# Kernel optimization log

Hardware: AMD Instinct MI355X
Metric: run time of the kernel (lower is better)

Reference implementation:

```python
import jax, jax.numpy as jnp
import numpy as np

B, S, D_IN, D_OUT = 4, 2048, 1024, 1024

def setup_inputs() -> dict:
    key = jax.random.key(0)
    k0, k1, k2, k3 = jax.random.split(key, 4)
    sc = 1.0 / np.sqrt(D_IN)
    return {
        "x": jax.random.normal(k0, (B, S, D_IN), dtype=jnp.float32),
        "wq": jax.random.normal(k1, (D_OUT, D_IN), dtype=jnp.float32) * sc,
        "wk": jax.random.normal(k2, (D_OUT, D_IN), dtype=jnp.float32) * sc,
        "wv": jax.random.normal(k3, (D_OUT, D_IN), dtype=jnp.float32) * sc,
    }

def reference(x, wq, wk, wv):
    # Linear (no bias): y = x @ W.T, W shaped [d_out, d_in]
    q = jnp.einsum("bsd,ed->bse", x, wq)
    k = jnp.einsum("bsd,ed->bse", x, wk)
    v = jnp.einsum("bsd,ed->bse", x, wv)
    scores = jnp.einsum("bqe,bke->bqk", q, k)  # [B,S,S]
    n = x.shape[1]
    causal = jnp.triu(jnp.ones((n, n), dtype=bool), k=1)  # True above diagonal -> masked
    scores = jnp.where(causal, -jnp.inf, scores)
    attn = jax.nn.softmax(scores / jnp.sqrt(jnp.asarray(k.shape[-1], scores.dtype)), axis=-1)
    # dropout p=0.0 -> identity
    return jnp.einsum("bqk,bke->bqe", attn, v)
```

## Files before the change

kernel.cpp:

```cpp
#include <hip/hip_runtime.h>

#define Bb 4
#define Ss 2048
#define Dd 1024

typedef unsigned short u16;
typedef __bf16 bf16x8 __attribute__((ext_vector_type(8)));
typedef float  f32x4  __attribute__((ext_vector_type(4)));

__device__ inline u16 f2bf(float f) {
  union { float f; unsigned u; } x; x.f = f;
  unsigned u = x.u;
  return (u16)((u + 0x7fffu + ((u >> 16) & 1u)) >> 16);
}

__device__ static inline void gl_lds16(const u16* g, u16* l) {
  __builtin_amdgcn_global_load_lds((__attribute__((address_space(1))) const void*)g,
                                   (__attribute__((address_space(3))) void*)l,
                                   16, 0, 0);
}

__global__ __launch_bounds__(256) void cast_kernel(const float* __restrict__ in,
                                                   u16* __restrict__ out, int n) {
  int i = (blockIdx.x * 256 + threadIdx.x) * 4;
  if (i >= n) return;
  float4 v = *(const float4*)(in + i);
  unsigned p0 = (unsigned)f2bf(v.x) | ((unsigned)f2bf(v.y) << 16);
  unsigned p1 = (unsigned)f2bf(v.z) | ((unsigned)f2bf(v.w) << 16);
  uint2 p; p.x = p0; p.y = p1;
  *(uint2*)(out + i) = p;
}

__global__ __launch_bounds__(256) void cast3_kernel(const float* __restrict__ w0,
                                                    const float* __restrict__ w1,
                                                    const float* __restrict__ w2,
                                                    u16* __restrict__ out) {
  const float* src = (blockIdx.y == 0) ? w0 : (blockIdx.y == 1) ? w1 : w2;
  u16* dst = out + (size_t)blockIdx.y * Dd * Dd;
  int i = (blockIdx.x * 256 + threadIdx.x) * 4;
  float4 v = *(const float4*)(src + i);
  unsigned p0 = (unsigned)f2bf(v.x) | ((unsigned)f2bf(v.y) << 16);
  unsigned p1 = (unsigned)f2bf(v.z) | ((unsigned)f2bf(v.w) << 16);
  uint2 p; p.x = p0; p.y = p1;
  *(uint2*)(dst + i) = p;
}

#define BM 128
#define BN 128
#define BK 32

__device__ inline void gemm_tile(const u16* __restrict__ A, int lda,
                                 const u16* __restrict__ Bp, int ldb,
                                 int kBeg, int kEnd,
                                 u16* lA, u16* lB, f32x4 acc[4][4]) {
  const int tid  = threadIdx.x;
  const int lane = tid & 63, wave = tid >> 6;
  const int quad = lane >> 4, r16 = lane & 15;
  const int wm = (wave & 1) * 64, wn = (wave >> 1) * 64;

  for (int k0 = kBeg; k0 < kEnd; k0 += BK) {
    __syncthreads();
#pragma unroll
    for (int q = 0; q < 2; q++) {
      int s = q * 256 + tid;
      int row = s >> 2, part = s & 3;
      gl_lds16(A + (size_t)row * lda + k0 + part * 8, lA + s * 8);
    }
#pragma unroll
    for (int q = 0; q < 2; q++) {
      int s = q * 256 + tid;
      int row = s >> 2, part = s & 3;
      gl_lds16(Bp + (size_t)row * ldb + k0 + part * 8, lB + s * 8);
    }
    __syncthreads();
    bf16x8 fa[4], fb[4];
#pragma unroll
    for (int t = 0; t < 4; t++)
      fa[t] = *(const bf16x8*)(lA + (wm + t * 16 + r16) * 32 + quad * 8);
#pragma unroll
    for (int t = 0; t < 4; t++)
      fb[t] = *(const bf16x8*)(lB + (wn + t * 16 + r16) * 32 + quad * 8);
#pragma unroll
    for (int tm = 0; tm < 4; tm++)
#pragma unroll
      for (int tn = 0; tn < 4; tn++)
        acc[tm][tn] = __builtin_amdgcn_mfma_f32_16x16x32_bf16(fa[tm], fb[tn],
                                                              acc[tm][tn], 0, 0, 0);
  }
}

__global__ __launch_bounds__(256) void qkv_gemm(const u16* __restrict__ xb,
                                                const u16* __restrict__ wb,
                                                u16* __restrict__ qkv) {
  __shared__ __align__(16) u16 lA[BM * 32];
  __shared__ __align__(16) u16 lB[BN * 32];
  const int zi = blockIdx.z;
  const int row0 = blockIdx.y * BM;
  const int col0 = blockIdx.x * BN;
  const u16* A  = xb + (size_t)row0 * Dd;
  const u16* Bp = wb + (size_t)zi * Dd * Dd + (size_t)col0 * Dd;
  f32x4 acc[4][4];
  const f32x4 zero = {0.f, 0.f, 0.f, 0.f};
#pragma unroll
  for (int tm = 0; tm < 4; tm++)
#pragma unroll
    for (int tn = 0; tn < 4; tn++) acc[tm][tn] = zero;

  gemm_tile(A, Dd, Bp, Dd, 0, Dd, lA, lB, acc);

  u16* out = qkv + (size_t)zi * ((size_t)Bb * Ss * Dd);
  const int lane = threadIdx.x & 63, wave = threadIdx.x >> 6;
  const int quad = lane >> 4, r16 = lane & 15;
  const int wm = (wave & 1) * 64, wn = (wave >> 1) * 64;
#pragma unroll
  for (int tm = 0; tm < 4; tm++)
#pragma unroll
    for (int tn = 0; tn < 4; tn++) {
      int rr = row0 + wm + tm * 16 + quad * 4;
      int cc = col0 + wn + tn * 16 + r16;
#pragma unroll
      for (int r = 0; r < 4; r++)
        out[(size_t)(rr + r) * Dd + cc] = f2bf(acc[tm][tn][r]);
    }
}

__global__ __launch_bounds__(256) void scores_gemm(const u16* __restrict__ qb,
                                                   const u16* __restrict__ kb,
                                                   u16* __restrict__ sc) {
  const int jt = blockIdx.x, it = blockIdx.y, b = blockIdx.z;
  if (jt > it) return;
  __shared__ __align__(16) u16 lA[BM * 32];
  __shared__ __align__(16) u16 lB[BN * 32];
  const u16* A  = qb + (size_t)b * Ss * Dd + (size_t)it * BM * Dd;
  const u16* Bp = kb + (size_t)b * Ss * Dd + (size_t)jt * BN * Dd;
  f32x4 acc[4][4];
  const f32x4 zero = {0.f, 0.f, 0.f, 0.f};
#pragma unroll
  for (int tm = 0; tm < 4; tm++)
#pragma unroll
    for (int tn = 0; tn < 4; tn++) acc[tm][tn] = zero;

  gemm_tile(A, Dd, Bp, Dd, 0, Dd, lA, lB, acc);

  u16* out = sc + (size_t)b * Ss * Ss;
  const int lane = threadIdx.x & 63, wave = threadIdx.x >> 6;
  const int quad = lane >> 4, r16 = lane & 15;
  const int wm = (wave & 1) * 64, wn = (wave >> 1) * 64;
#pragma unroll
  for (int tm = 0; tm < 4; tm++)
#pragma unroll
    for (int tn = 0; tn < 4; tn++) {
      int rr = it * BM + wm + tm * 16 + quad * 4;
      int cc = jt * BN + wn + tn * 16 + r16;
#pragma unroll
      for (int r = 0; r < 4; r++) {
        u16 v = (cc <= rr + r) ? f2bf(__expf(acc[tm][tn][r] * 0.03125f)) : (u16)0;
        out[(size_t)(rr + r) * Ss + cc] = v;
      }
    }
}

__global__ __launch_bounds__(256) void rowsum_kernel(const u16* __restrict__ sc,
                                                     float* __restrict__ invl) {
  const int wave = threadIdx.x >> 6, lane = threadIdx.x & 63;
  const int rid = blockIdx.x * 4 + wave;
  const int b = rid >> 11, i = rid & 2047;
  const u16* row = sc + (size_t)b * Ss * Ss + (size_t)i * Ss;
  const int n8 = ((i >> 7) + 1) * 128;
  float s = 0.f;
  for (int j = lane * 8; j < n8; j += 512) {
    bf16x8 v = *(const bf16x8*)(row + j);
#pragma unroll
    for (int t = 0; t < 8; t++) s += (float)v[t];
  }
  for (int o = 32; o; o >>= 1) s += __shfl_xor(s, o);
  if (lane == 0) invl[rid] = 1.f / s;
}

__global__ __launch_bounds__(256) void transpose_v(const u16* __restrict__ vb,
                                                   u16* __restrict__ vt) {
  const int b = blockIdx.z;
  const int s0 = blockIdx.x * 64;
  const int e0 = blockIdx.y * 64;
  __shared__ __align__(16) u16 t[64][72];
  const int tid = threadIdx.x;
  const u16* src = vb + (size_t)b * Ss * Dd;
#pragma unroll
  for (int g = tid; g < 512; g += 256) {
    int row = g >> 3, part = g & 7;
    uint4 v = *(const uint4*)(src + (size_t)(s0 + row) * Dd + e0 + part * 8);
    const u16* pv = (const u16*)&v;
#pragma unroll
    for (int j = 0; j < 8; j++) t[part * 8 + j][row] = pv[j];
  }
  __syncthreads();
  u16* dst = vt + (size_t)b * Dd * Ss;
#pragma unroll
  for (int g = tid; g < 512; g += 256) {
    int e = g >> 3, part = g & 7;
    uint4 v = *(const uint4*)(&t[e][part * 8]);
    *(uint4*)(dst + (size_t)(e0 + e) * Ss + s0 + part * 8) = v;
  }
}

__global__ __launch_bounds__(256) void pv_gemm(const u16* __restrict__ sc,
                                               const u16* __restrict__ vt,
                                               const float* __restrict__ invl,
                                               float* __restrict__ out) {
  const int idx = blockIdx.x;
  const int it = 15 - (idx >> 5);
  const int rem = idx & 31;
  const int col0 = (rem & 7) * BN;
  const int b = rem >> 3;
  const int row0 = it * BM;
  __shared__ __align__(16) u16 lA[BM * 32];
  __shared__ __align__(16) u16 lB[BN * 32];
  const u16* A  = sc + (size_t)b * Ss * Ss + (size_t)row0 * Ss;
  const u16* Bp = vt + (size_t)b * Dd * Ss + (size_t)col0 * Ss;
  f32x4 acc[4][4];
  const f32x4 zero = {0.f, 0.f, 0.f, 0.f};
#pragma unroll
  for (int tm = 0; tm < 4; tm++)
#pragma unroll
    for (int tn = 0; tn < 4; tn++) acc[tm][tn] = zero;

  gemm_tile(A, Ss, Bp, Ss, 0, row0 + BM, lA, lB, acc);

  float* o = out + (size_t)b * Ss * Dd;
  const float* il = invl + (size_t)b * Ss;
  const int lane = threadIdx.x & 63, wave = threadIdx.x >> 6;
  const int quad = lane >> 4, r16 = lane & 15;
  const int wm = (wave & 1) * 64, wn = (wave >> 1) * 64;
#pragma unroll
  for (int tm = 0; tm < 4; tm++) {
    int rbase = row0 + wm + tm * 16 + quad * 4;
    float s0 = il[rbase], s1 = il[rbase + 1], s2 = il[rbase + 2], s3 = il[rbase + 3];
#pragma unroll
    for (int tn = 0; tn < 4; tn++) {
      int cc = col0 + wn + tn * 16 + r16;
      o[(size_t)(rbase + 0) * Dd + cc] = acc[tm][tn][0] * s0;
      o[(size_t)(rbase + 1) * Dd + cc] = acc[tm][tn][1] * s1;
      o[(size_t)(rbase + 2) * Dd + cc] = acc[tm][tn][2] * s2;
      o[(size_t)(rbase + 3) * Dd + cc] = acc[tm][tn][3] * s3;
    }
  }
}

extern "C" void kernel_launch(void* const* d_in, const int* in_sizes, int n_in,
                              void* d_out, int out_size, void* d_ws, size_t ws_size,
                              hipStream_t stream) {
  const float* x  = (const float*)d_in[0];
  const float* wq = (const float*)d_in[1];
  const float* wk = (const float*)d_in[2];
  const float* wv = (const float*)d_in[3];
  float* out = (float*)d_out;
  char* ws = (char*)d_ws;
  if (ws_size < 106987520u) return;

  u16* qkv  = (u16*)(ws);
  u16* sc   = (u16*)(ws + 50331648u);
  u16* xb   = (u16*)(ws + 83886080u);
  u16* vt   = xb;
  u16* wb   = (u16*)(ws + 100663296u);
  float* invl = (float*)(ws + 106954752u);

  const size_t nQ = (size_t)Bb * Ss * Dd;

  cast_kernel<<<8192, 256, 0, stream>>>(x, xb, (int)nQ);
  cast3_kernel<<<dim3(1024, 3), 256, 0, stream>>>(wq, wk, wv, wb);

  qkv_gemm<<<dim3(Dd / BN, (Bb * Ss) / BM, 3), 256, 0, stream>>>(xb, wb, qkv);
  scores_gemm<<<dim3(Ss / BN, Ss / BM, Bb), 256, 0, stream>>>(qkv, qkv + nQ, sc);
  rowsum_kernel<<<(Bb * Ss) / 4, 256, 0, stream>>>(sc, invl);
  transpose_v<<<dim3(Ss / 64, Dd / 64, Bb), 256, 0, stream>>>(qkv + 2 * nQ, vt);
  pv_gemm<<<512, 256, 0, stream>>>(sc, vt, invl, out);
}
```

Before: 273.7 us.

## Fuse cast kernels, fold rowsum and V-transpose into scores kernel, XCD-aware remap

Merges the x and weight cast kernels into one launch. The rowsum kernel is removed: row sums are now accumulated in the scores epilogue with shuffles and atomicAdd, after a memset of the sum buffer. The V transpose now runs as extra blocks inside the scores launch, and only the lower-triangular score tiles are launched. qkv_gemm and scores tiles are remapped so neighbouring tiles land on the same XCD for L2 reuse. This cuts launch count and avoids re-reading the scores matrix, at the cost of atomics and a per-element reciprocal in pv_gemm.

```diff
diff --git a/kernel.cpp b/kernel.cpp
--- a/kernel.cpp
+++ b/kernel.cpp
@@ -13,6 +13,10 @@
   unsigned u = x.u;
   return (u16)((u + 0x7fffu + ((u >> 16) & 1u)) >> 16);
 }
+__device__ inline float bf2f(u16 h) {
+  union { unsigned u; float f; } x; x.u = ((unsigned)h) << 16;
+  return x.f;
+}
 
 __device__ static inline void gl_lds16(const u16* g, u16* l) {
   __builtin_amdgcn_global_load_lds((__attribute__((address_space(1))) const void*)g,
@@ -20,24 +24,24 @@
                                    16, 0, 0);
 }
 
-__global__ __launch_bounds__(256) void cast_kernel(const float* __restrict__ in,
-                                                   u16* __restrict__ out, int n) {
-  int i = (blockIdx.x * 256 + threadIdx.x) * 4;
-  if (i >= n) return;
-  float4 v = *(const float4*)(in + i);
-  unsigned p0 = (unsigned)f2bf(v.x) | ((unsigned)f2bf(v.y) << 16);
-  unsigned p1 = (unsigned)f2bf(v.z) | ((unsigned)f2bf(v.w) << 16);
-  uint2 p; p.x = p0; p.y = p1;
-  *(uint2*)(out + i) = p;
-}
-
-__global__ __launch_bounds__(256) void cast3_kernel(const float* __restrict__ w0,
-                                                    const float* __restrict__ w1,
-                                                    const float* __restrict__ w2,
-                                                    u16* __restrict__ out) {
-  const float* src = (blockIdx.y == 0) ? w0 : (blockIdx.y == 1) ? w1 : w2;
-  u16* dst = out + (size_t)blockIdx.y * Dd * Dd;
-  int i = (blockIdx.x * 256 + threadIdx.x) * 4;
+__global__ __launch_bounds__(256) void cast_all(const float* __restrict__ x,
+                                                const float* __restrict__ wq,
+                                                const float* __restrict__ wk,
+                                                const float* __restrict__ wv,
+                                                u16* __restrict__ xb,
+                                                u16* __restrict__ wb) {
+  int id = blockIdx.x;
+  const float* src; u16* dst; int off;
+  if (id < 8192) {
+    src = x; dst = xb; off = id * 1024;
+  } else {
+    int wi = id - 8192;
+    int w = wi >> 10;
+    src = (w == 0) ? wq : (w == 1) ? wk : wv;
+    dst = wb + (size_t)w * Dd * Dd;
+    off = (wi & 1023) * 1024;
+  }
+  int i = off + threadIdx.x * 4;
   float4 v = *(const float4*)(src + i);
   unsigned p0 = (unsigned)f2bf(v.x) | ((unsigned)f2bf(v.y) << 16);
   unsigned p1 = (unsigned)f2bf(v.z) | ((unsigned)f2bf(v.w) << 16);
@@ -92,11 +96,17 @@
 __global__ __launch_bounds__(256) void qkv_gemm(const u16* __restrict__ xb,
                                                 const u16* __restrict__ wb,
                                                 u16* __restrict__ qkv) {
-  __shared__ __align__(16) u16 lA[BM * 32];
-  __shared__ __align__(16) u16 lB[BN * 32];
-  const int zi = blockIdx.z;
-  const int row0 = blockIdx.y * BM;
-  const int col0 = blockIdx.x * BN;
+  __shared__ __align__(16) u16 shmem[8192];
+  u16* lA = shmem;
+  u16* lB = shmem + 4096;
+  const int id  = blockIdx.x;
+  const int xcd = id & 7, j = id >> 3;
+  const int xt  = j & 7;
+  const int yl  = (j >> 3) & 7;
+  const int zi  = j >> 6;
+  const int y   = xcd * 8 + yl;
+  const int row0 = y * BM;
+  const int col0 = xt * BN;
   const u16* A  = xb + (size_t)row0 * Dd;
   const u16* Bp = wb + (size_t)zi * Dd * Dd + (size_t)col0 * Dd;
   f32x4 acc[4][4];
@@ -124,13 +134,55 @@
     }
 }
 
-__global__ __launch_bounds__(256) void scores_gemm(const u16* __restrict__ qb,
-                                                   const u16* __restrict__ kb,
-                                                   u16* __restrict__ sc) {
-  const int jt = blockIdx.x, it = blockIdx.y, b = blockIdx.z;
-  if (jt > it) return;
-  __shared__ __align__(16) u16 lA[BM * 32];
-  __shared__ __align__(16) u16 lB[BN * 32];
+__global__ __launch_bounds__(256) void scores_fused(const u16* __restrict__ qb,
+                                                    const u16* __restrict__ kb,
+                                                    const u16* __restrict__ vb,
+                                                    u16* __restrict__ sc,
+                                                    u16* __restrict__ vt,
+                                                    float* __restrict__ lsum) {
+  __shared__ __align__(16) u16 shmem[8192];
+  const int id = blockIdx.x;
+  const int tid = threadIdx.x;
+
+  if (id >= 544) {
+    const int t2 = id - 544;
+    const int b = t2 >> 7, rem = t2 & 127;
+    const int e = rem >> 3, g = rem & 7;
+    const u16* src = vb + (size_t)b * Ss * Dd;
+    u16* dst = vt + (size_t)b * Dd * Ss;
+    u16 (*t)[72] = (u16(*)[72])shmem;
+    for (int q4 = 0; q4 < 4; q4++) {
+      int s0 = (g * 4 + q4) * 64, e0 = e * 64;
+      if (q4) __syncthreads();
+#pragma unroll
+      for (int gg = tid; gg < 512; gg += 256) {
+        int row = gg >> 3, part = gg & 7;
+        uint4 v = *(const uint4*)(src + (size_t)(s0 + row) * Dd + e0 + part * 8);
+        const u16* pv = (const u16*)&v;
+#pragma unroll
+        for (int jj = 0; jj < 8; jj++) t[part * 8 + jj][row] = pv[jj];
+      }
+      __syncthreads();
+#pragma unroll
+      for (int gg = tid; gg < 512; gg += 256) {
+        int ee = gg >> 3, part = gg & 7;
+        uint4 v = *(const uint4*)(&t[ee][part * 8]);
+        *(uint4*)(dst + (size_t)(e0 + ee) * Ss + s0 + part * 8) = v;
+      }
+    }
+    return;
+  }
+
+  const int xcd = id & 7, j = id >> 3;
+  const int b = j / 17, tloc = j - b * 17;
+  const int t = xcd * 17 + tloc;
+  int it = (int)((sqrtf(8.f * (float)t + 1.f) - 1.f) * 0.5f);
+  while ((it + 1) * (it + 2) / 2 <= t) it++;
+  while (it * (it + 1) / 2 > t) it--;
+  const int jt = t - it * (it + 1) / 2;
+
+  u16* lA = shmem;
+  u16* lB = shmem + 4096;
   const u16* A  = qb + (size_t)b * Ss * Dd + (size_t)it * BM * Dd;
   const u16* Bp = kb + (size_t)b * Ss * Dd + (size_t)jt * BN * Dd;
   f32x4 acc[4][4];
@@ -143,78 +195,57 @@
   gemm_tile(A, Dd, Bp, Dd, 0, Dd, lA, lB, acc);
 
   u16* out = sc + (size_t)b * Ss * Ss;
-  const int lane = threadIdx.x & 63, wave = threadIdx.x >> 6;
+  float* lr = lsum + (size_t)b * Ss;
+  const int lane = tid & 63, wave = tid >> 6;
   const int quad = lane >> 4, r16 = lane & 15;
   const int wm = (wave & 1) * 64, wn = (wave >> 1) * 64;
 #pragma unroll
-  for (int tm = 0; tm < 4; tm++)
+  for (int tm = 0; tm < 4; tm++) {
+    float psum[4] = {0.f, 0.f, 0.f, 0.f};
 #pragma unroll
     for (int tn = 0; tn < 4; tn++) {
       int rr = it * BM + wm + tm * 16 + quad * 4;
       int cc = jt * BN + wn + tn * 16 + r16;
 #pragma unroll
       for (int r = 0; r < 4; r++) {
-        u16 v = (cc <= rr + r) ? f2bf(__expf(acc[tm][tn][r] * 0.03125f)) : (u16)0;
-        out[(size_t)(rr + r) * Ss + cc] = v;
+        float p = 0.f;
+        u16 h = 0;
+        if (cc <= rr + r) {
+          h = f2bf(__expf(acc[tm][tn][r] * 0.03125f));
+          p = bf2f(h);
+        }
+        out[(size_t)(rr + r) * Ss + cc] = h;
+        psum[r] += p;
       }
     }
-}
-
-__global__ __launch_bounds__(256) void rowsum_kernel(const u16* __restrict__ sc,
-                                                     float* __restrict__ invl) {
-  const int wave = threadIdx.x >> 6, lane = threadIdx.x & 63;
-  const int rid = blockIdx.x * 4 + wave;
-  const int b = rid >> 11, i = rid & 2047;
-  const u16* row = sc + (size_t)b * Ss * Ss + (size_t)i * Ss;
-  const int n8 = ((i >> 7) + 1) * 128;
-  float s = 0.f;
-  for (int j = lane * 8; j < n8; j += 512) {
-    bf16x8 v = *(const bf16x8*)(row + j);
-#pragma unroll
-    for (int t = 0; t < 8; t++) s += (float)v[t];
-  }
-  for (int o = 32; o; o >>= 1) s += __shfl_xor(s, o);
-  if (lane == 0) invl[rid] = 1.f / s;
-}
-
-__global__ __launch_bounds__(256) void transpose_v(const u16* __restrict__ vb,
-                                                   u16* __restrict__ vt) {
-  const int b = blockIdx.z;
-  const int s0 = blockIdx.x * 64;
-  const int e0 = blockIdx.y * 64;
-  __shared__ __align__(16) u16 t[64][72];
-  const int tid = threadIdx.x;
-  const u16* src = vb + (size_t)b * Ss * Dd;
-#pragma unroll
-  for (int g = tid; g < 512; g += 256) {
-    int row = g >> 3, part = g & 7;
-    uint4 v = *(const uint4*)(src + (size_t)(s0 + row) * Dd + e0 + part * 8);
-    const u16* pv = (const u16*)&v;
-#pragma unroll
-    for (int j = 0; j < 8; j++) t[part * 8 + j][row] = pv[j];
-  }
-  __syncthreads();
-  u16* dst = vt + (size_t)b * Dd * Ss;
-#pragma unroll
-  for (int g = tid; g < 512; g += 256) {
-    int e = g >> 3, part = g & 7;
-    uint4 v = *(const uint4*)(&t[e][part * 8]);
-    *(uint4*)(dst + (size_t)(e0 + e) * Ss + s0 + part * 8) = v;
+#pragma unroll
+    for (int r = 0; r < 4; r++) {
+      float s = psum[r];
+      s += __shfl_xor(s, 1);
+      s += __shfl_xor(s, 2);
+      s += __shfl_xor(s, 4);
+      s += __shfl_xor(s, 8);
+      if (r16 == 0) {
+        int row = it * BM + wm + tm * 16 + quad * 4 + r;
+        atomicAdd(&lr[row], s);
+      }
+    }
   }
 }
 
 __global__ __launch_bounds__(256) void pv_gemm(const u16* __restrict__ sc,
                                                const u16* __restrict__ vt,
-                                               const float* __restrict__ invl,
+                                               const float* __restrict__ lsum,
                                                float* __restrict__ out) {
+  __shared__ __align__(16) u16 shmem[8192];
+  u16* lA = shmem;
+  u16* lB = shmem + 4096;
   const int idx = blockIdx.x;
   const int it = 15 - (idx >> 5);
   const int rem = idx & 31;
   const int col0 = (rem & 7) * BN;
   const int b = rem >> 3;
   const int row0 = it * BM;
-  __shared__ __align__(16) u16 lA[BM * 32];
-  __shared__ __align__(16) u16 lB[BN * 32];
   const u16* A  = sc + (size_t)b * Ss * Ss + (size_t)row0 * Ss;
   const u16* Bp = vt + (size_t)b * Dd * Ss + (size_t)col0 * Ss;
   f32x4 acc[4][4];
@@ -227,14 +258,15 @@
   gemm_tile(A, Ss, Bp, Ss, 0, row0 + BM, lA, lB, acc);
 
   float* o = out + (size_t)b * Ss * Dd;
-  const float* il = invl + (size_t)b * Ss;
+  const float* lr = lsum + (size_t)b * Ss;
   const int lane = threadIdx.x & 63, wave = threadIdx.x >> 6;
   const int quad = lane >> 4, r16 = lane & 15;
   const int wm = (wave & 1) * 64, wn = (wave >> 1) * 64;
 #pragma unroll
   for (int tm = 0; tm < 4; tm++) {
     int rbase = row0 + wm + tm * 16 + quad * 4;
-    float s0 = il[rbase], s1 = il[rbase + 1], s2 = il[rbase + 2], s3 = il[rbase + 3];
+    float s0 = 1.f / lr[rbase], s1 = 1.f / lr[rbase + 1];
+    float s2 = 1.f / lr[rbase + 2], s3 = 1.f / lr[rbase + 3];
 #pragma unroll
     for (int tn = 0; tn < 4; tn++) {
       int cc = col0 + wn + tn * 16 + r16;
@@ -262,16 +294,13 @@
   u16* xb   = (u16*)(ws + 83886080u);
   u16* vt   = xb;
   u16* wb   = (u16*)(ws + 100663296u);
-  float* invl = (float*)(ws + 106954752u);
+  float* lsum = (float*)(ws + 106954752u);
 
   const size_t nQ = (size_t)Bb * Ss * Dd;
 
-  cast_kernel<<<8192, 256, 0, stream>>>(x, xb, (int)nQ);
-  cast3_kernel<<<dim3(1024, 3), 256, 0, stream>>>(wq, wk, wv, wb);
-
-  qkv_gemm<<<dim3(Dd / BN, (Bb * Ss) / BM, 3), 256, 0, stream>>>(xb, wb, qkv);
-  scores_gemm<<<dim3(Ss / BN, Ss / BM, Bb), 256, 0, stream>>>(qkv, qkv + nQ, sc);
-  rowsum_kernel<<<(Bb * Ss) / 4, 256, 0, stream>>>(sc, invl);
-  transpose_v<<<dim3(Ss / 64, Dd / 64, Bb), 256, 0, stream>>>(qkv + 2 * nQ, vt);
-  pv_gemm<<<512, 256, 0, stream>>>(sc, vt, invl, out);
-}
+  hipMemsetAsync(lsum, 0, Bb * Ss * sizeof(float), stream);
+  cast_all<<<11264, 256, 0, stream>>>(x, wq, wk, wv, xb, wb);
+  qkv_gemm<<<1536, 256, 0, stream>>>(xb, wb, qkv);
+  scores_fused<<<1056, 256, 0, stream>>>(qkv, qkv + nQ, qkv + 2 * nQ, sc, vt, lsum);
+  pv_gemm<<<512, 256, 0, stream>>>(sc, vt, lsum, out);
+}
```

New measurement: 239.4 us. 12.5% less time.
